# Kernel tuning notes

Hardware: AMD Instinct MI355X
Metric: run time of the kernel (lower is better)

Reference implementation:

```python
import math
import jax, jax.numpy as jnp
import numpy as np

DIM = 256
B, S = 4, 4096

def setup_inputs() -> dict:
    key = jax.random.key(0)
    k1, k2, k3, k4 = jax.random.split(key, 4)
    x = jax.random.normal(k1, (B, S, DIM), dtype=jnp.float32)
    W = jax.random.normal(k2, (3 * DIM, DIM), dtype=jnp.float32) * 0.02
    b = jax.random.normal(k3, (3 * DIM,), dtype=jnp.float32) * 0.02
    attention_mask = jax.random.randint(k4, (B, 1, S), 0, 2, dtype=jnp.int32)
    return {"x": x, "W": W, "b": b, "attention_mask": attention_mask}

def reference(x, W, b, attention_mask):
    # qkv projection: Linear(dim, 3*dim) -> x @ W^T + b
    qkv = jnp.einsum("bsd,ed->bse", x, W) + b  # [B,S,3*DIM]
    q, k, v = jnp.split(qkv, 3, axis=-1)
    # NOTE: module computes q @ v^T (not q @ k^T) -- faithful to source
    scores = jnp.einsum("bqd,bkd->bqk", q, v) / math.sqrt(DIM)  # [B,S,S]
    scores = jnp.where(attention_mask == 0, -jnp.inf, scores)
    attn = jax.nn.softmax(scores, axis=-1)
    # dropout in eval mode -> identity
    out = jnp.einsum("bqk,bkd->bqd", attn, v)  # [B,S,DIM]
    return out
```

## Files before the change

### kernel.cpp

```cpp
#include <hip/hip_runtime.h>
#include <hip/hip_bf16.h>

#define DIMC 256
#define NB 4
#define NS 4096
#define KT 64
#define NTILES (NS / KT)
#define VS_ELEMS (KT * DIMC)

typedef __attribute__((ext_vector_type(4))) float f32x4;
typedef __attribute__((ext_vector_type(8))) short bf16x8;

__device__ __forceinline__ ushort f2bf(float f) {
  __hip_bfloat16 h = __float2bfloat16(f);
  return *reinterpret_cast<ushort*>(&h);
}
__device__ __forceinline__ float bf2f(ushort h) {
  uint u = ((uint)h) << 16;
  float f;
  __builtin_memcpy(&f, &u, 4);
  return f;
}

__device__ __forceinline__ void gload16(const ushort* g, ushort* l) {
  __builtin_amdgcn_global_load_lds(
      (const __attribute__((address_space(1))) unsigned int*)g,
      (__attribute__((address_space(3))) unsigned int*)l,
      16, 0, 0);
}

__global__ void wsplit_kernel(const float* __restrict__ W, ushort* __restrict__ Whl) {
  const int col = blockIdx.x;
  const int k = threadIdx.x;
  const int srcrow = (col < 256) ? col : (col + 256);
  float f = W[(size_t)srcrow * 256 + k];
  ushort h = f2bf(f);
  Whl[(size_t)col * 256 + k] = h;
  Whl[131072 + (size_t)col * 256 + k] = f2bf(f - bf2f(h));
}

__global__ __launch_bounds__(256) void qv_proj_kernel(
    const float* __restrict__ x, const ushort* __restrict__ Whl,
    const float* __restrict__ bias,
    ushort* __restrict__ qb, ushort* __restrict__ vb, ushort* __restrict__ vtb)
{
  const int tid  = threadIdx.x;
  const int w    = tid >> 6;
  const int lane = tid & 63;
  const int l15  = lane & 15;
  const int g    = (lane >> 4) & 3;
  const int r0   = blockIdx.x << 6;
  const int colbase = w << 7;

  __shared__ ushort olds[64 * 520];

  f32x4 acc[4][8];
  #pragma unroll
  for (int rt = 0; rt < 4; ++rt)
    #pragma unroll
    for (int ct = 0; ct < 8; ++ct) { acc[rt][ct].x=0.f; acc[rt][ct].y=0.f; acc[rt][ct].z=0.f; acc[rt][ct].w=0.f; }

  #pragma unroll 1
  for (int st = 0; st < 8; ++st) {
    bf16x8 xh[4], xl[4];
    #pragma unroll
    for (int rt = 0; rt < 4; ++rt) {
      const float* p = x + (size_t)(r0 + rt * 16 + l15) * DIMC + st * 32 + g * 8;
      float4 f0 = *(const float4*)p;
      float4 f1 = *(const float4*)(p + 4);
      union { bf16x8 v; ushort u[8]; } uh, ul;
      #pragma unroll
      for (int e = 0; e < 8; ++e) {
        float fe = (e < 4) ? ((const float*)&f0)[e] : ((const float*)&f1)[e - 4];
        ushort h = f2bf(fe);
        uh.u[e] = h;
        ul.u[e] = f2bf(fe - bf2f(h));
      }
      xh[rt] = uh.v;
      xl[rt] = ul.v;
    }
    #pragma unroll
    for (int ct = 0; ct < 8; ++ct) {
      const ushort* wp = Whl + (size_t)(colbase + ct * 16 + l15) * 256 + st * 32 + g * 8;
      bf16x8 wh = *(const bf16x8*)wp;
      bf16x8 wl = *(const bf16x8*)(wp + 131072);
      #pragma unroll
      for (int rt = 0; rt < 4; ++rt) {
        acc[rt][ct] = __builtin_amdgcn_mfma_f32_16x16x32_bf16(xh[rt], wh, acc[rt][ct], 0, 0, 0);
        acc[rt][ct] = __builtin_amdgcn_mfma_f32_16x16x32_bf16(xl[rt], wh, acc[rt][ct], 0, 0, 0);
        acc[rt][ct] = __builtin_amdgcn_mfma_f32_16x16x32_bf16(xh[rt], wl, acc[rt][ct], 0, 0, 0);
      }
    }
  }

  const float qscale = (colbase < 256) ? 0.0625f : 1.0f;
  #pragma unroll
  for (int ct = 0; ct < 8; ++ct) {
    const int col = colbase + ct * 16 + l15;
    const float bv = bias[(col < 256) ? col : (col + 256)];
    #pragma unroll
    for (int rt = 0; rt < 4; ++rt) {
      #pragma unroll
      for (int r = 0; r < 4; ++r)
        olds[(rt * 16 + 4 * g + r) * 520 + col] = f2bf((acc[rt][ct][r] + bv) * qscale);
    }
  }
  __syncthreads();

  #pragma unroll
  for (int i = 0; i < 16; ++i) {
    int task = tid + i * 256;
    int row = task >> 6, ch = task & 63;
    uint4 d = *(const uint4*)&olds[row * 520 + ch * 8];
    if (ch < 32) *(uint4*)&qb[(size_t)(r0 + row) * DIMC + ch * 8] = d;
    else         *(uint4*)&vb[(size_t)(r0 + row) * DIMC + (ch - 32) * 8] = d;
  }
  const int bbp = r0 >> 12;
  const int s0  = r0 & (NS - 1);
  const int vcol = tid;
  #pragma unroll
  for (int o = 0; o < 8; ++o) {
    union { uint4 v; ushort u[8]; } pk;
    #pragma unroll
    for (int j = 0; j < 8; ++j)
      pk.u[j] = olds[(o * 8 + j) * 520 + 256 + vcol];
    *(uint4*)&vtb[((size_t)(bbp * DIMC + vcol)) * NS + s0 + o * 8] = pk.v;
  }
}

__global__ void mask_pack_kernel(const int* __restrict__ mask, uint* __restrict__ pm32) {
  int t = blockIdx.x * 64 + threadIdx.x;
  int b = t >> 7;
  int kt = (t >> 1) & 63;
  int kh = t & 1;
  const int* mrow = mask + b * NS + kt * 64 + kh * 32;
  uint wd = 0;
  for (int g = 0; g < 4; ++g)
    for (int ntl = 0; ntl < 2; ++ntl)
      for (int r = 0; r < 4; ++r)
        if (mrow[ntl * 16 + 4 * g + r] != 0) wd |= 1u << (8 * g + ntl * 4 + r);
  pm32[t] = wd;
}

__global__ __launch_bounds__(512, 2) void attn_kernel(
    const ushort* __restrict__ qb, const ushort* __restrict__ vb,
    const ushort* __restrict__ vtb, const uint* __restrict__ pm32,
    float* __restrict__ out)
{
  const int tid  = threadIdx.x;
  const int w    = tid >> 6;
  const int lane = tid & 63;
  const int l15  = lane & 15;
  const int g    = (lane >> 4) & 3;
  const int kh   = w & 1;
  const int pq   = w >> 1;

  const int qrow0 = blockIdx.x << 6;
  const int bb    = qrow0 >> 12;

  extern __shared__ __align__(16) char smem[];
  uint*   pmlds = (uint*)smem;
  ushort* vs0  = (ushort*)(smem + 1024);
  ushort* vs1  = vs0 + VS_ELEMS;
  ushort* vt0  = vs1 + VS_ELEMS;
  ushort* vt1  = vt0 + VS_ELEMS;
  ushort* psb  = vt1 + VS_ELEMS;

  const int qrow = qrow0 + (pq << 4) + l15;
  bf16x8 qreg[8];
  #pragma unroll
  for (int st = 0; st < 8; ++st)
    qreg[st] = *(const bf16x8*)&qb[(size_t)qrow * DIMC + ((st * 4 + g) << 3)];

  if (tid < 128) pmlds[tid] = pm32[(bb << 7) + tid];

  auto stage = [&](int kt, ushort* vsN, ushort* vtN) {
    const ushort* vbase = vb + ((size_t)(bb * NS + kt * KT)) * DIMC;
    #pragma unroll
    for (int i = 0; i < 4; ++i) {
      int rr0 = (w << 3) + (i << 1);
      int row = rr0 + (lane >> 5);
      int cs  = lane & 31;
      gload16(vbase + row * DIMC + ((cs ^ (row & 7)) << 3), vsN + (rr0 << 8));
    }
    #pragma unroll
    for (int i = 0; i < 4; ++i) {
      int d0 = i << 6;
      int dim = (d0 + lane) ^ ((w & 3) << 1);
      gload16(vtb + ((size_t)(bb * DIMC + dim)) * NS + kt * KT + (w << 3),
              vtN + ((w << 8) + d0) * 8);
    }
  };

  stage(0, vs0, vt0);
  asm volatile("s_waitcnt vmcnt(0)" ::: "memory");
  __syncthreads();

  f32x4 acc_o[16];
  #pragma unroll
  for (int nt = 0; nt < 16; ++nt) { acc_o[nt].x=0.f; acc_o[nt].y=0.f; acc_o[nt].z=0.f; acc_o[nt].w=0.f; }
  float m_s = -30.f;
  float l_s = 0.f;

  ushort* psw = psb + w * (16 * 40);

  auto tile_body = [&](int kt, const ushort* vs_, const ushort* vt_,
                       ushort* vsN, ushort* vtN) {
    if (kt + 1 < NTILES) stage(kt + 1, vsN, vtN);

    f32x4 sacc[2];
    sacc[0].x=0.f; sacc[0].y=0.f; sacc[0].z=0.f; sacc[0].w=0.f;
    sacc[1] = sacc[0];
    __builtin_amdgcn_s_setprio(1);
    #pragma unroll
    for (int st = 0; st < 8; ++st) {
      #pragma unroll
      for (int ntl = 0; ntl < 2; ++ntl) {
        int key = ((kh << 1) + ntl) * 16 + l15;
        bf16x8 af = *(const bf16x8*)&vs_[(key * 32 + ((st * 4 + g) ^ (key & 7))) * 8];
        sacc[ntl] = __builtin_amdgcn_mfma_f32_16x16x32_bf16(af, qreg[st], sacc[ntl], 0, 0, 0);
      }
    }
    __builtin_amdgcn_s_setprio(0);

    uint mybits = (pmlds[(kt << 1) + kh] >> (g << 3)) & 0xffu;

    float v[8];
    #pragma unroll
    for (int ntl = 0; ntl < 2; ++ntl)
      #pragma unroll
      for (int r = 0; r < 4; ++r)
        v[ntl * 4 + r] = (mybits & (1u << (ntl * 4 + r))) ? sacc[ntl][r] : -1e30f;
    float tm = fmaxf(fmaxf(fmaxf(v[0], v[1]), fmaxf(v[2], v[3])),
                     fmaxf(fmaxf(v[4], v[5]), fmaxf(v[6], v[7])));
    tm = fmaxf(tm, __shfl_xor(tm, 16));
    tm = fmaxf(tm, __shfl_xor(tm, 32));
    float mo = m_s;
    float mn = fmaxf(mo, tm);
    float p[8];
    #pragma unroll
    for (int j = 0; j < 8; ++j) p[j] = __expf(v[j] - mn);
    float rs = ((p[0] + p[1]) + (p[2] + p[3])) + ((p[4] + p[5]) + (p[6] + p[7]));
    rs += __shfl_xor(rs, 16);
    rs += __shfl_xor(rs, 32);
    if (__any((int)(mn > mo))) {
      float sc = __expf(mo - mn);
      m_s = mn;
      l_s = l_s * sc + rs;
      #pragma unroll
      for (int nt = 0; nt < 16; ++nt) acc_o[nt] *= sc;
    } else {
      l_s += rs;
    }

    #pragma unroll
    for (int ntl = 0; ntl < 2; ++ntl) {
      uint2 pk;
      pk.x = (uint)f2bf(p[ntl*4+0]) | ((uint)f2bf(p[ntl*4+1]) << 16);
      pk.y = (uint)f2bf(p[ntl*4+2]) | ((uint)f2bf(p[ntl*4+3]) << 16);
      *(uint2*)&psw[l15 * 40 + ntl * 16 + 4 * g] = pk;
    }

    bf16x8 pa = *(const bf16x8*)&psw[l15 * 40 + (g << 3)];
    const int kc = (kh << 2) + g;
    __builtin_amdgcn_s_setprio(1);
    #pragma unroll
    for (int nt = 0; nt < 16; ++nt) {
      bf16x8 vf = *(const bf16x8*)&vt_[((kc << 8) + ((nt * 16 + l15) ^ ((kc & 3) << 1))) * 8];
      acc_o[nt] = __builtin_amdgcn_mfma_f32_16x16x32_bf16(vf, pa, acc_o[nt], 0, 0, 0);
    }
    __builtin_amdgcn_s_setprio(0);

    asm volatile("s_waitcnt vmcnt(0)" ::: "memory");
    __syncthreads();
  };

  for (int kt2 = 0; kt2 < NTILES; kt2 += 2) {
    tile_body(kt2,     vs0, vt0, vs1, vt1);
    tile_body(kt2 + 1, vs1, vt1, vs0, vt0);
  }

  f32x4* accS = (f32x4*)(smem + 1024);
  float*  mlS = (float*)(smem + 1024 + 65536);
  if (kh) {
    #pragma unroll
    for (int nt = 0; nt < 16; ++nt)
      accS[((pq << 6) + lane) * 16 + nt] = acc_o[nt];
    mlS[((pq << 6) + lane) * 2]     = m_s;
    mlS[((pq << 6) + lane) * 2 + 1] = l_s;
  }
  __syncthreads();
  if (!kh) {
    float mB = mlS[((pq << 6) + lane) * 2];
    float lB = mlS[((pq << 6) + lane) * 2 + 1];
    float m  = fmaxf(m_s, mB);
    float eA = __expf(m_s - m);
    float eB = __expf(mB - m);
    float inv = 1.f / (l_s * eA + lB * eB);
    float fA = eA * inv;
    float fB = eB * inv;
    const size_t obase = (size_t)(qrow0 + (pq << 4) + l15) * DIMC + 4 * g;
    #pragma unroll
    for (int nt = 0; nt < 16; ++nt) {
      f32x4 oB = accS[((pq << 6) + lane) * 16 + nt];
      f32x4 o = acc_o[nt] * fA + oB * fB;
      *(float4*)&out[obase + nt * 16] = *(float4*)&o;
    }
  }
}

extern "C" void kernel_launch(void* const* d_in, const int* in_sizes, int n_in,
                              void* d_out, int out_size, void* d_ws, size_t ws_size,
                              hipStream_t stream) {
  const float* x    = (const float*)d_in[0];
  const float* W    = (const float*)d_in[1];
  const float* bias = (const float*)d_in[2];
  const int*   mask = (const int*)d_in[3];
  float* out = (float*)d_out;

  const size_t n = (size_t)NB * NS * DIMC;
  ushort* qb  = (ushort*)d_ws;
  ushort* vb  = qb + n;
  ushort* vtb = vb + n;
  uint* pm32 = (uint*)(vtb + n);
  ushort* Whl = (ushort*)(pm32 + 512);

  wsplit_kernel<<<512, 256, 0, stream>>>(W, Whl);
  mask_pack_kernel<<<8, 64, 0, stream>>>(mask, pm32);
  qv_proj_kernel<<<(NB * NS) / 64, 256, 0, stream>>>(x, Whl, bias, qb, vb, vtb);

  const int smem_bytes = 1024 + 4 * VS_ELEMS * 2 + 8 * 16 * 40 * 2;
  attn_kernel<<<(NB * NS) / 64, 512, smem_bytes, stream>>>(qb, vb, vtb, pm32, out);
}
```

Measured before the change: 174.6 us.

## Process 128 query rows per block with split-key halves and a merge kernel

```diff
diff --git a/kernel.cpp b/kernel.cpp
--- a/kernel.cpp
+++ b/kernel.cpp
@@ -5,7 +5,6 @@
 #define NB 4
 #define NS 4096
 #define KT 64
-#define NTILES (NS / KT)
 #define VS_ELEMS (KT * DIMC)
 
 typedef __attribute__((ext_vector_type(4))) float f32x4;
@@ -145,7 +144,8 @@
 __global__ __launch_bounds__(512, 2) void attn_kernel(
     const ushort* __restrict__ qb, const ushort* __restrict__ vb,
     const ushort* __restrict__ vtb, const uint* __restrict__ pm32,
-    float* __restrict__ out)
+    float* __restrict__ outA, float* __restrict__ opB,
+    float* __restrict__ mlA, float* __restrict__ mlB)
 {
   const int tid  = threadIdx.x;
   const int w    = tid >> 6;
@@ -155,8 +155,14 @@
   const int kh   = w & 1;
   const int pq   = w >> 1;
 
-  const int qrow0 = blockIdx.x << 6;
+  const int s     = blockIdx.x & 1;
+  const int qb128 = blockIdx.x >> 1;
+  const int qrow0 = qb128 << 7;
   const int bb    = qrow0 >> 12;
+  const int koff  = s << 11;
+
+  float* opart = s ? opB : outA;
+  float* mlp   = s ? mlB : mlA;
 
   extern __shared__ __align__(16) char smem[];
   uint*   pmlds = (uint*)smem;
@@ -166,16 +172,19 @@
   ushort* vt1  = vt0 + VS_ELEMS;
   ushort* psb  = vt1 + VS_ELEMS;
 
-  const int qrow = qrow0 + (pq << 4) + l15;
-  bf16x8 qreg[8];
-  #pragma unroll
-  for (int st = 0; st < 8; ++st)
-    qreg[st] = *(const bf16x8*)&qb[(size_t)qrow * DIMC + ((st * 4 + g) << 3)];
+  bf16x8 qreg[2][8];
+  #pragma unroll
+  for (int qt = 0; qt < 2; ++qt) {
+    const int qrow = qrow0 + (pq << 5) + (qt << 4) + l15;
+    #pragma unroll
+    for (int st = 0; st < 8; ++st)
+      qreg[qt][st] = *(const bf16x8*)&qb[(size_t)qrow * DIMC + ((st * 4 + g) << 3)];
+  }
 
   if (tid < 128) pmlds[tid] = pm32[(bb << 7) + tid];
 
   auto stage = [&](int kt, ushort* vsN, ushort* vtN) {
-    const ushort* vbase = vb + ((size_t)(bb * NS + kt * KT)) * DIMC;
+    const ushort* vbase = vb + ((size_t)(bb * NS + koff + kt * KT)) * DIMC;
     #pragma unroll
     for (int i = 0; i < 4; ++i) {
       int rr0 = (w << 3) + (i << 1);
@@ -187,7 +196,7 @@
     for (int i = 0; i < 4; ++i) {
       int d0 = i << 6;
       int dim = (d0 + lane) ^ ((w & 3) << 1);
-      gload16(vtb + ((size_t)(bb * DIMC + dim)) * NS + kt * KT + (w << 3),
+      gload16(vtb + ((size_t)(bb * DIMC + dim)) * NS + koff + kt * KT + (w << 3),
               vtN + ((w << 8) + d0) * 8);
     }
   };
@@ -196,78 +205,91 @@
   asm volatile("s_waitcnt vmcnt(0)" ::: "memory");
   __syncthreads();
 
-  f32x4 acc_o[16];
-  #pragma unroll
-  for (int nt = 0; nt < 16; ++nt) { acc_o[nt].x=0.f; acc_o[nt].y=0.f; acc_o[nt].z=0.f; acc_o[nt].w=0.f; }
-  float m_s = -30.f;
-  float l_s = 0.f;
-
-  ushort* psw = psb + w * (16 * 40);
+  f32x4 acc_o[2][16];
+  #pragma unroll
+  for (int qt = 0; qt < 2; ++qt)
+    #pragma unroll
+    for (int nt = 0; nt < 16; ++nt) { acc_o[qt][nt].x=0.f; acc_o[qt][nt].y=0.f; acc_o[qt][nt].z=0.f; acc_o[qt][nt].w=0.f; }
+  float m_s[2] = {-30.f, -30.f};
+  float l_s[2] = {0.f, 0.f};
+
+  ushort* psw = psb + w * (32 * 40);
 
   auto tile_body = [&](int kt, const ushort* vs_, const ushort* vt_,
                        ushort* vsN, ushort* vtN) {
-    if (kt + 1 < NTILES) stage(kt + 1, vsN, vtN);
-
-    f32x4 sacc[2];
-    sacc[0].x=0.f; sacc[0].y=0.f; sacc[0].z=0.f; sacc[0].w=0.f;
-    sacc[1] = sacc[0];
+    if (kt + 1 < 32) stage(kt + 1, vsN, vtN);
+
+    f32x4 sacc[2][2];
+    #pragma unroll
+    for (int qt = 0; qt < 2; ++qt) {
+      sacc[qt][0].x=0.f; sacc[qt][0].y=0.f; sacc[qt][0].z=0.f; sacc[qt][0].w=0.f;
+      sacc[qt][1] = sacc[qt][0];
+    }
     __builtin_amdgcn_s_setprio(1);
     #pragma unroll
     for (int st = 0; st < 8; ++st) {
+      const int key0 = (kh << 5) + l15;
+      bf16x8 af0 = *(const bf16x8*)&vs_[(key0 * 32 + ((st * 4 + g) ^ (key0 & 7))) * 8];
+      const int key1 = key0 + 16;
+      bf16x8 af1 = *(const bf16x8*)&vs_[(key1 * 32 + ((st * 4 + g) ^ (key1 & 7))) * 8];
+      #pragma unroll
+      for (int qt = 0; qt < 2; ++qt) {
+        sacc[qt][0] = __builtin_amdgcn_mfma_f32_16x16x32_bf16(af0, qreg[qt][st], sacc[qt][0], 0, 0, 0);
+        sacc[qt][1] = __builtin_amdgcn_mfma_f32_16x16x32_bf16(af1, qreg[qt][st], sacc[qt][1], 0, 0, 0);
+      }
+    }
+    __builtin_amdgcn_s_setprio(0);
+
+    const int ktg = (s << 5) + kt;
+    uint mybits = (pmlds[(ktg << 1) + kh] >> (g << 3)) & 0xffu;
+
+    #pragma unroll
+    for (int qt = 0; qt < 2; ++qt) {
+      float v[8];
+      #pragma unroll
+      for (int ntl = 0; ntl < 2; ++ntl)
+        #pragma unroll
+        for (int r = 0; r < 4; ++r)
+          v[ntl * 4 + r] = (mybits & (1u << (ntl * 4 + r))) ? sacc[qt][ntl][r] : -1e30f;
+      float tm = fmaxf(fmaxf(fmaxf(v[0], v[1]), fmaxf(v[2], v[3])),
+                       fmaxf(fmaxf(v[4], v[5]), fmaxf(v[6], v[7])));
+      tm = fmaxf(tm, __shfl_xor(tm, 16));
+      tm = fmaxf(tm, __shfl_xor(tm, 32));
+      float mo = m_s[qt];
+      float mn = fmaxf(mo, tm);
+      float p[8];
+      #pragma unroll
+      for (int j = 0; j < 8; ++j) p[j] = __expf(v[j] - mn);
+      float rs = ((p[0] + p[1]) + (p[2] + p[3])) + ((p[4] + p[5]) + (p[6] + p[7]));
+      rs += __shfl_xor(rs, 16);
+      rs += __shfl_xor(rs, 32);
+      if (__any((int)(mn > mo))) {
+        float sc = __expf(mo - mn);
+        m_s[qt] = mn;
+        l_s[qt] = l_s[qt] * sc + rs;
+        #pragma unroll
+        for (int nt = 0; nt < 16; ++nt) acc_o[qt][nt] *= sc;
+      } else {
+        l_s[qt] += rs;
+      }
       #pragma unroll
       for (int ntl = 0; ntl < 2; ++ntl) {
-        int key = ((kh << 1) + ntl) * 16 + l15;
-        bf16x8 af = *(const bf16x8*)&vs_[(key * 32 + ((st * 4 + g) ^ (key & 7))) * 8];
-        sacc[ntl] = __builtin_amdgcn_mfma_f32_16x16x32_bf16(af, qreg[st], sacc[ntl], 0, 0, 0);
-      }
-    }
-    __builtin_amdgcn_s_setprio(0);
-
-    uint mybits = (pmlds[(kt << 1) + kh] >> (g << 3)) & 0xffu;
-
-    float v[8];
-    #pragma unroll
-    for (int ntl = 0; ntl < 2; ++ntl)
-      #pragma unroll
-      for (int r = 0; r < 4; ++r)
-        v[ntl * 4 + r] = (mybits & (1u << (ntl * 4 + r))) ? sacc[ntl][r] : -1e30f;
-    float tm = fmaxf(fmaxf(fmaxf(v[0], v[1]), fmaxf(v[2], v[3])),
-                     fmaxf(fmaxf(v[4], v[5]), fmaxf(v[6], v[7])));
-    tm = fmaxf(tm, __shfl_xor(tm, 16));
-    tm = fmaxf(tm, __shfl_xor(tm, 32));
-    float mo = m_s;
-    float mn = fmaxf(mo, tm);
-    float p[8];
-    #pragma unroll
-    for (int j = 0; j < 8; ++j) p[j] = __expf(v[j] - mn);
-    float rs = ((p[0] + p[1]) + (p[2] + p[3])) + ((p[4] + p[5]) + (p[6] + p[7]));
-    rs += __shfl_xor(rs, 16);
-    rs += __shfl_xor(rs, 32);
-    if (__any((int)(mn > mo))) {
-      float sc = __expf(mo - mn);
-      m_s = mn;
-      l_s = l_s * sc + rs;
-      #pragma unroll
-      for (int nt = 0; nt < 16; ++nt) acc_o[nt] *= sc;
-    } else {
-      l_s += rs;
-    }
-
-    #pragma unroll
-    for (int ntl = 0; ntl < 2; ++ntl) {
-      uint2 pk;
-      pk.x = (uint)f2bf(p[ntl*4+0]) | ((uint)f2bf(p[ntl*4+1]) << 16);
-      pk.y = (uint)f2bf(p[ntl*4+2]) | ((uint)f2bf(p[ntl*4+3]) << 16);
-      *(uint2*)&psw[l15 * 40 + ntl * 16 + 4 * g] = pk;
-    }
-
-    bf16x8 pa = *(const bf16x8*)&psw[l15 * 40 + (g << 3)];
+        uint2 pk;
+        pk.x = (uint)f2bf(p[ntl*4+0]) | ((uint)f2bf(p[ntl*4+1]) << 16);
+        pk.y = (uint)f2bf(p[ntl*4+2]) | ((uint)f2bf(p[ntl*4+3]) << 16);
+        *(uint2*)&psw[((qt << 4) + l15) * 40 + ntl * 16 + 4 * g] = pk;
+      }
+    }
+
+    bf16x8 pa0 = *(const bf16x8*)&psw[l15 * 40 + (g << 3)];
+    bf16x8 pa1 = *(const bf16x8*)&psw[(16 + l15) * 40 + (g << 3)];
     const int kc = (kh << 2) + g;
     __builtin_amdgcn_s_setprio(1);
     #pragma unroll
     for (int nt = 0; nt < 16; ++nt) {
       bf16x8 vf = *(const bf16x8*)&vt_[((kc << 8) + ((nt * 16 + l15) ^ ((kc & 3) << 1))) * 8];
-      acc_o[nt] = __builtin_amdgcn_mfma_f32_16x16x32_bf16(vf, pa, acc_o[nt], 0, 0, 0);
+      acc_o[0][nt] = __builtin_amdgcn_mfma_f32_16x16x32_bf16(vf, pa0, acc_o[0][nt], 0, 0, 0);
+      acc_o[1][nt] = __builtin_amdgcn_mfma_f32_16x16x32_bf16(vf, pa1, acc_o[1][nt], 0, 0, 0);
     }
     __builtin_amdgcn_s_setprio(0);
 
@@ -275,38 +297,73 @@
     __syncthreads();
   };
 
-  for (int kt2 = 0; kt2 < NTILES; kt2 += 2) {
+  for (int kt2 = 0; kt2 < 32; kt2 += 2) {
     tile_body(kt2,     vs0, vt0, vs1, vt1);
     tile_body(kt2 + 1, vs1, vt1, vs0, vt0);
   }
 
   f32x4* accS = (f32x4*)(smem + 1024);
-  float*  mlS = (float*)(smem + 1024 + 65536);
+  float*  mlS = (float*)(smem + 1024 + 131072);
   if (kh) {
     #pragma unroll
-    for (int nt = 0; nt < 16; ++nt)
-      accS[((pq << 6) + lane) * 16 + nt] = acc_o[nt];
-    mlS[((pq << 6) + lane) * 2]     = m_s;
-    mlS[((pq << 6) + lane) * 2 + 1] = l_s;
+    for (int qt = 0; qt < 2; ++qt) {
+      #pragma unroll
+      for (int nt = 0; nt < 16; ++nt)
+        accS[(((pq << 1) + qt) * 64 + lane) * 16 + nt] = acc_o[qt][nt];
+      if (g == 0) {
+        mlS[(((pq << 1) + qt) * 16 + l15) * 2]     = m_s[qt];
+        mlS[(((pq << 1) + qt) * 16 + l15) * 2 + 1] = l_s[qt];
+      }
+    }
   }
   __syncthreads();
   if (!kh) {
-    float mB = mlS[((pq << 6) + lane) * 2];
-    float lB = mlS[((pq << 6) + lane) * 2 + 1];
-    float m  = fmaxf(m_s, mB);
-    float eA = __expf(m_s - m);
-    float eB = __expf(mB - m);
-    float inv = 1.f / (l_s * eA + lB * eB);
-    float fA = eA * inv;
-    float fB = eB * inv;
-    const size_t obase = (size_t)(qrow0 + (pq << 4) + l15) * DIMC + 4 * g;
-    #pragma unroll
-    for (int nt = 0; nt < 16; ++nt) {
-      f32x4 oB = accS[((pq << 6) + lane) * 16 + nt];
-      f32x4 o = acc_o[nt] * fA + oB * fB;
-      *(float4*)&out[obase + nt * 16] = *(float4*)&o;
-    }
-  }
+    #pragma unroll
+    for (int qt = 0; qt < 2; ++qt) {
+      float mB = mlS[(((pq << 1) + qt) * 16 + l15) * 2];
+      float lB = mlS[(((pq << 1) + qt) * 16 + l15) * 2 + 1];
+      float m12 = fmaxf(m_s[qt], mB);
+      float eA = __expf(m_s[qt] - m12);
+      float eB = __expf(mB - m12);
+      float l12 = l_s[qt] * eA + lB * eB;
+      const int qrow = qrow0 + (pq << 5) + (qt << 4) + l15;
+      const size_t obase = (size_t)qrow * DIMC + 4 * g;
+      #pragma unroll
+      for (int nt = 0; nt < 16; ++nt) {
+        f32x4 oB = accS[(((pq << 1) + qt) * 64 + lane) * 16 + nt];
+        f32x4 o = acc_o[qt][nt] * eA + oB * eB;
+        *(float4*)&opart[obase + nt * 16] = *(float4*)&o;
+      }
+      if (g == 0) {
+        mlp[(size_t)qrow * 2]     = m12;
+        mlp[(size_t)qrow * 2 + 1] = l12;
+      }
+    }
+  }
+}
+
+__global__ __launch_bounds__(256) void merge_kernel(
+    float* __restrict__ outA, const float* __restrict__ opB,
+    const float* __restrict__ mlA, const float* __restrict__ mlB)
+{
+  int id = blockIdx.x * 256 + threadIdx.x;
+  int row = id >> 6;
+  int c = (id & 63) << 2;
+  float mA = mlA[(size_t)row * 2], lA = mlA[(size_t)row * 2 + 1];
+  float mB = mlB[(size_t)row * 2], lB = mlB[(size_t)row * 2 + 1];
+  float m = fmaxf(mA, mB);
+  float eA = __expf(mA - m), eB = __expf(mB - m);
+  float inv = 1.f / (lA * eA + lB * eB);
+  float fA = eA * inv, fB = eB * inv;
+  size_t o = (size_t)row * DIMC + c;
+  float4 a = *(const float4*)&outA[o];
+  float4 b = *(const float4*)&opB[o];
+  float4 r;
+  r.x = a.x * fA + b.x * fB;
+  r.y = a.y * fA + b.y * fB;
+  r.z = a.z * fA + b.z * fB;
+  r.w = a.w * fA + b.w * fB;
+  *(float4*)&outA[o] = r;
 }
 
 extern "C" void kernel_launch(void* const* d_in, const int* in_sizes, int n_in,
@@ -324,11 +381,15 @@
   ushort* vtb = vb + n;
   uint* pm32 = (uint*)(vtb + n);
   ushort* Whl = (ushort*)(pm32 + 512);
+  float* opB = (float*)(Whl + 262144);
+  float* mlA = opB + n;
+  float* mlB = mlA + 2 * (NB * NS);
 
   wsplit_kernel<<<512, 256, 0, stream>>>(W, Whl);
   mask_pack_kernel<<<8, 64, 0, stream>>>(mask, pm32);
   qv_proj_kernel<<<(NB * NS) / 64, 256, 0, stream>>>(x, Whl, bias, qb, vb, vtb);
 
-  const int smem_bytes = 1024 + 4 * VS_ELEMS * 2 + 8 * 16 * 40 * 2;
-  attn_kernel<<<(NB * NS) / 64, 512, smem_bytes, stream>>>(qb, vb, vtb, pm32, out);
-}
+  const int smem_bytes = 1024 + 4 * VS_ELEMS * 2 + 8 * 32 * 40 * 2;
+  attn_kernel<<<256, 512, smem_bytes, stream>>>(qb, vb, vtb, pm32, out, opB, mlA, mlB);
+  merge_kernel<<<(NB * NS * DIMC / 4) / 256, 256, 0, stream>>>(out, opB, mlA, mlB);
+}
```

Result: slower. 438.2 us (+151.0%).
